# Kernel optimization log

Measured on AMD Instinct MI355X. Metric: run time of the kernel, lower is better.

Reference implementation:

```python
import jax, jax.numpy as jnp
import numpy as np

N = 100000
E = 1600000
IN_FT = 128
OUT_FT = 128
SELF_LOOP_FILL = 3.0


def setup_inputs() -> dict:
    key = jax.random.key(0)
    k1, k2, k3, k4 = jax.random.split(key, 4)
    seq = jax.random.normal(k1, (N, IN_FT), dtype=jnp.float32)
    edge_index = jax.random.randint(k2, (2, E), 0, N, dtype=jnp.int64)
    edge_weight = jax.random.uniform(k3, (E,), dtype=jnp.float32)
    # xavier_uniform for Linear(in_ft, out_ft): W shape [out_ft, in_ft]
    limit = float(np.sqrt(6.0 / (IN_FT + OUT_FT)))
    W = jax.random.uniform(k4, (OUT_FT, IN_FT), dtype=jnp.float32, minval=-limit, maxval=limit)
    return {"seq": seq, "edge_weight": edge_weight, "W": W, "edge_index": edge_index}


def reference(seq, edge_weight, W, edge_index):
    n = seq.shape[0]
    # dropout with drop_prob=0.0 is identity; fc_1: x = seq @ W^T
    x = seq @ W.T  # [N, out_ft]
    # add self loops with fill_value=3.0
    loops = jnp.arange(n, dtype=edge_index.dtype)
    row = jnp.concatenate([edge_index[0], loops])
    col = jnp.concatenate([edge_index[1], loops])
    w = jnp.concatenate([edge_weight, jnp.full((n,), SELF_LOOP_FILL, dtype=edge_weight.dtype)])
    # symmetric normalization: deg^-1/2 [row] * w * deg^-1/2 [col]
    deg = jax.ops.segment_sum(w, row, num_segments=n)
    deg_inv_sqrt = jnp.where(deg > 0, jax.lax.rsqrt(deg), jnp.zeros_like(deg))
    norm = deg_inv_sqrt[row] * w * deg_inv_sqrt[col]
    # sparse aggregation: out[r] += norm_e * x[c]
    out = jax.ops.segment_sum(norm[:, None] * x[col], row, num_segments=n)
    return jax.nn.relu(out)
```

## Files before the change

### kernel.cpp

```cpp
#include <hip/hip_runtime.h>


#define TPB 256
#define NBROWS 256
#define BCAP 4608
#define RCAP 48
#define EPB 2048
#define GPW 4

typedef __attribute__((ext_vector_type(8))) short s16x8;
typedef __attribute__((ext_vector_type(4))) float f32x4;

__device__ inline unsigned bf16rne(float x) {
    unsigned u = __float_as_uint(x);
    u += 0x7FFF + ((u >> 16) & 1);
    return u >> 16;
}

__global__ void k_init(int* __restrict__ cursor, int m,
                       const float* __restrict__ W, unsigned* __restrict__ wb) {
    int i = blockIdx.x * TPB + threadIdx.x;
    if (i < m) cursor[i] = 0;
    if (i < 2048) {
        int j = i >> 4, g = i & 15;
        const float* src = W + j * 128 + g * 8;
        float4 f0 = *(const float4*)src;
        float4 f1 = *(const float4*)(src + 4);
        uint4 pk;
        pk.x = bf16rne(f0.x) | (bf16rne(f0.y) << 16);
        pk.y = bf16rne(f0.z) | (bf16rne(f0.w) << 16);
        pk.z = bf16rne(f1.x) | (bf16rne(f1.y) << 16);
        pk.w = bf16rne(f1.z) | (bf16rne(f1.w) << 16);
        ((uint4*)wb)[i] = pk;
    }
}

__global__ __launch_bounds__(TPB) void k_partition(const int* __restrict__ ei,
                                                   const float* __restrict__ ew,
                                                   int* __restrict__ cursor,
                                                   int2* __restrict__ part,
                                                   int e, int nb) {
    __shared__ int hist[512];
    __shared__ int chunk[512];
    int t = threadIdx.x;
    hist[t] = 0; hist[t + 256] = 0;
    chunk[t] = 0; chunk[t + 256] = 0;
    __syncthreads();

    long base = (long)blockIdx.x * EPB;
    for (int j = 0; j < EPB / 256; ++j) {
        long idx = base + j * 256 + t;
        if (idx < e) atomicAdd(&hist[ei[idx] >> 8], 1);
    }
    __syncthreads();
    for (int b = t; b < nb; b += TPB) {
        int h = hist[b];
        chunk[b] = (h > 0) ? atomicAdd(&cursor[b * 16], h) : 0;
    }
    __syncthreads();
    hist[t] = 0; hist[t + 256] = 0;
    __syncthreads();
    for (int j = 0; j < EPB / 256; ++j) {
        long idx = base + j * 256 + t;
        if (idx < e) {
            int r = ei[idx];
            int c = ei[e + idx];
            float w = ew[idx];
            int b = r >> 8;
            int rank = atomicAdd(&hist[b], 1);
            int dst = chunk[b] + rank;
            if (dst < BCAP)
                part[(long)b * BCAP + dst] =
                    make_int2(((r & 255) << 17) | c, __float_as_int(w));
        }
    }
}

__global__ __launch_bounds__(TPB) void k_build_prescale(const int2* __restrict__ part,
                                                        const int* __restrict__ cursor,
                                                        unsigned* __restrict__ slotsG,
                                                        float2* __restrict__ dc,
                                                        const float* __restrict__ seq,
                                                        unsigned* __restrict__ xb, int n) {
    __shared__ unsigned lslot[NBROWS * RCAP];
    __shared__ int rowcnt[NBROWS];
    __shared__ float rdis[NBROWS];
    int b = blockIdx.x, t = threadIdx.x;
    rowcnt[t] = 0;
    for (int j = t; j < NBROWS * RCAP; j += TPB) lslot[j] = 0;
    __syncthreads();

    int m = cursor[b * 16]; if (m > BCAP) m = BCAP;
    for (int i = t; i < m; i += TPB) {
        int2 en = part[(long)b * BCAP + i];
        int rl = ((unsigned)en.x) >> 17;
        int c  = en.x & 0x1FFFF;
        float w = __int_as_float(en.y);
        int pos = atomicAdd(&rowcnt[rl], 1);
        if (pos < RCAP) {
            int q = (int)(w * 32768.0f);
            if (q > 32767) q = 32767;
            lslot[rl * RCAP + pos] = ((unsigned)q << 17) | (unsigned)c;
        }
    }
    __syncthreads();

    int node = b * NBROWS + t;
    float di = 0.0f;
    if (node < n) {
        int rc = rowcnt[t]; if (rc > RCAP) rc = RCAP;
        float s = 0.0f;
        for (int k = 0; k < rc; ++k)
            s += ((float)(lslot[t * RCAP + k] >> 17) + 0.5f) * (1.0f / 32768.0f);
        di = rsqrtf(3.0f + s);
        dc[node] = make_float2(di, __int_as_float(rc));
    }
    rdis[t] = di;
    for (int j = t; j < NBROWS * RCAP; j += TPB)
        slotsG[(long)b * (NBROWS * RCAP) + j] = lslot[j];
    __syncthreads();

    long pbase = (long)b * NBROWS * 64;
    long plim = (long)n * 64;
    for (int j = t; j < NBROWS * 64; j += TPB) {
        long pidx = pbase + j;
        if (pidx < plim) {
            float d = rdis[j >> 6];
            float2 s2 = ((const float2*)seq)[pidx];
            xb[pidx] = bf16rne(d * s2.x) | (bf16rne(d * s2.y) << 16);
        }
    }
}

__global__ __launch_bounds__(TPB) void k_gather_gemm(const unsigned* __restrict__ xb,
                                                     const unsigned* __restrict__ slotsG,
                                                     const float2* __restrict__ dc,
                                                     const unsigned* __restrict__ wb,
                                                     float* __restrict__ out, int n) {
    __shared__ short ylds[16 * 128];
    int t = threadIdx.x;
    int wave = t >> 6, lane = t & 63;

    int node0 = blockIdx.x * (4 * GPW) + wave * GPW;

    float di[GPW];
    int   m[GPW];
    int   cl[GPW];
    float vl[GPW];
    float2 acc[GPW];
    int mmax = 0;

#pragma unroll
    for (int q = 0; q < GPW; ++q) {
        int node = node0 + q;
        bool has = (node < n);
        float2 d = has ? dc[node] : make_float2(0.0f, __int_as_float(0));
        di[q] = d.x;
        m[q] = __float_as_int(d.y);
        if (m[q] > mmax) mmax = m[q];
        unsigned s = (has && lane < m[q]) ? slotsG[(long)node * RCAP + lane] : 0u;
        int c = (int)(s & 0x1FFFF); if (c > n - 1) c = n - 1;
        cl[q] = c;
        vl[q] = (lane < m[q]) ? ((float)(s >> 17) + 0.5f) * (1.0f / 32768.0f) : 0.0f;
        unsigned u = has ? xb[(long)node * 64 + lane] : 0u;
        acc[q].x = 3.0f * __uint_as_float(u << 16);
        acc[q].y = 3.0f * __uint_as_float(u & 0xFFFF0000u);
    }

    unsigned xva[GPW], xvb[GPW], xvc[GPW];
    float    va[GPW],  vb[GPW],  vc[GPW];

#pragma unroll
    for (int q = 0; q < GPW; ++q) {
        int c = __shfl(cl[q], 0);
        va[q] = __shfl(vl[q], 0);
        xva[q] = xb[(long)c * 64 + lane];
    }
#pragma unroll
    for (int q = 0; q < GPW; ++q) {
        int c = __shfl(cl[q], 1);
        vb[q] = __shfl(vl[q], 1);
        xvb[q] = xb[(long)c * 64 + lane];
    }

    for (int p = 0; p < mmax; p += 3) {
#pragma unroll
        for (int q = 0; q < GPW; ++q) {
            int c = __shfl(cl[q], p + 2);
            vc[q] = __shfl(vl[q], p + 2);
            xvc[q] = xb[(long)c * 64 + lane];
        }
#pragma unroll
        for (int q = 0; q < GPW; ++q) {
            acc[q].x = fmaf(va[q], __uint_as_float(xva[q] << 16), acc[q].x);
            acc[q].y = fmaf(va[q], __uint_as_float(xva[q] & 0xFFFF0000u), acc[q].y);
        }
#pragma unroll
        for (int q = 0; q < GPW; ++q) {
            int c = __shfl(cl[q], p + 3);
            va[q] = __shfl(vl[q], p + 3);
            xva[q] = xb[(long)c * 64 + lane];
        }
#pragma unroll
        for (int q = 0; q < GPW; ++q) {
            acc[q].x = fmaf(vb[q], __uint_as_float(xvb[q] << 16), acc[q].x);
            acc[q].y = fmaf(vb[q], __uint_as_float(xvb[q] & 0xFFFF0000u), acc[q].y);
        }
#pragma unroll
        for (int q = 0; q < GPW; ++q) {
            int c = __shfl(cl[q], p + 4);
            vb[q] = __shfl(vl[q], p + 4);
            xvb[q] = xb[(long)c * 64 + lane];
        }
#pragma unroll
        for (int q = 0; q < GPW; ++q) {
            acc[q].x = fmaf(vc[q], __uint_as_float(xvc[q] << 16), acc[q].x);
            acc[q].y = fmaf(vc[q], __uint_as_float(xvc[q] & 0xFFFF0000u), acc[q].y);
        }
    }

    int quad = lane >> 4, l15 = lane & 15;
    s16x8 bfr[2][4];
#pragma unroll
    for (int h = 0; h < 2; ++h)
#pragma unroll
        for (int kc = 0; kc < 4; ++kc)
            bfr[h][kc] = ((const s16x8*)wb)[((wave * 2 + h) * 16 + l15) * 16 + kc * 4 + quad];

#pragma unroll
    for (int q = 0; q < GPW; ++q) {
        int r = wave * GPW + q;
        unsigned pkv = bf16rne(di[q] * acc[q].x) | (bf16rne(di[q] * acc[q].y) << 16);
        ((unsigned*)ylds)[r * 64 + ((((lane >> 2) ^ r) & 15) << 2) + (lane & 3)] = pkv;
    }
    __syncthreads();

    f32x4 acc2[2];
    acc2[0] = (f32x4){0.0f, 0.0f, 0.0f, 0.0f};
    acc2[1] = (f32x4){0.0f, 0.0f, 0.0f, 0.0f};

#pragma unroll
    for (int kc = 0; kc < 4; ++kc) {
        int gA = kc * 4 + quad;
        s16x8 a = *(const s16x8*)&ylds[l15 * 128 + ((gA ^ l15) << 3)];
        acc2[0] = __builtin_amdgcn_mfma_f32_16x16x32_bf16(a, bfr[0][kc], acc2[0], 0, 0, 0);
        acc2[1] = __builtin_amdgcn_mfma_f32_16x16x32_bf16(a, bfr[1][kc], acc2[1], 0, 0, 0);
    }

    long base = (long)blockIdx.x * 16;
#pragma unroll
    for (int h = 0; h < 2; ++h) {
        int ct = wave * 2 + h;
#pragma unroll
        for (int i = 0; i < 4; ++i) {
            long gr = base + quad * 4 + i;
            if (gr < n)
                out[gr * 128 + ct * 16 + l15] = fmaxf(acc2[h][i], 0.0f);
        }
    }
}

extern "C" void kernel_launch(void* const* d_in, const int* in_sizes, int n_in,
                              void* d_out, int out_size, void* d_ws, size_t ws_size,
                              hipStream_t stream) {
    const float* seq = (const float*)d_in[0];
    const float* ew  = (const float*)d_in[1];
    const float* W   = (const float*)d_in[2];
    const int*   ei  = (const int*)d_in[3];
    float* out = (float*)d_out;

    int n = in_sizes[0] / 128;
    int e = in_sizes[1];
    int nb = (n + NBROWS - 1) / NBROWS;

    char* w8 = (char*)d_ws;
    unsigned* xb   = (unsigned*)w8;
    size_t off = (size_t)n * 64 * 4;
    int2* part     = (int2*)(w8 + off);
    off += (size_t)nb * BCAP * 8;
    unsigned* slotsG = (unsigned*)(w8 + off);
    off += (size_t)nb * NBROWS * RCAP * 4;
    int* cursor    = (int*)(w8 + off);
    off += (size_t)nb * 16 * 4;
    float2* dc     = (float2*)(w8 + off);
    off += (size_t)n * 8;
    unsigned* wb   = (unsigned*)(w8 + off);

    k_init          <<<(nb * 16 + TPB - 1) / TPB, TPB, 0, stream>>>(cursor, nb * 16, W, wb);
    k_partition     <<<(e + EPB - 1) / EPB, TPB, 0, stream>>>(ei, ew, cursor, part, e, nb);
    k_build_prescale<<<nb, TPB, 0, stream>>>(part, cursor, slotsG, dc, seq, xb, n);
    k_gather_gemm   <<<(n + 4 * GPW - 1) / (4 * GPW), TPB, 0, stream>>>(xb, slotsG, dc, wb, out, n);
}
```

Measured before the change: 280.9 us.

## Replace two-level bucket partition with direct global-atomic scatter into per-row slots

Removes the bucket histogram/partition pass and the shared-memory slot build. Each edge now does a global atomicAdd on a per-row counter and writes its packed slot straight into a per-row RCAP array. A new wave-per-node kernel reduces the degree with shuffles and prescales seq into bf16. The change cuts one kernel launch and one round-trip through the intermediate partition buffer, at the cost of many contended global atomics and scattered writes. Slot ordering within a row also becomes nondeterministic.

```diff
diff --git a/kernel.cpp b/kernel.cpp
--- a/kernel.cpp
+++ b/kernel.cpp
@@ -2,10 +2,7 @@
 
 
 #define TPB 256
-#define NBROWS 256
-#define BCAP 4608
 #define RCAP 48
-#define EPB 2048
 #define GPW 4
 
 typedef __attribute__((ext_vector_type(8))) short s16x8;
@@ -17,11 +14,15 @@
     return u >> 16;
 }
 
-__global__ void k_init(int* __restrict__ cursor, int m,
-                       const float* __restrict__ W, unsigned* __restrict__ wb) {
-    int i = blockIdx.x * TPB + threadIdx.x;
-    if (i < m) cursor[i] = 0;
-    if (i < 2048) {
+__global__ __launch_bounds__(TPB) void k_scatter(const int* __restrict__ ei,
+                                                 const float* __restrict__ ew,
+                                                 int* __restrict__ rowcnt,
+                                                 unsigned* __restrict__ slotsG,
+                                                 const float* __restrict__ W,
+                                                 unsigned* __restrict__ wb, int e) {
+    int t = threadIdx.x;
+    if (blockIdx.x < 8) {
+        int i = blockIdx.x * TPB + t;
         int j = i >> 4, g = i & 15;
         const float* src = W + j * 128 + g * 8;
         float4 f0 = *(const float4*)src;
@@ -33,103 +34,43 @@
         pk.w = bf16rne(f1.z) | (bf16rne(f1.w) << 16);
         ((uint4*)wb)[i] = pk;
     }
-}
-
-__global__ __launch_bounds__(TPB) void k_partition(const int* __restrict__ ei,
-                                                   const float* __restrict__ ew,
-                                                   int* __restrict__ cursor,
-                                                   int2* __restrict__ part,
-                                                   int e, int nb) {
-    __shared__ int hist[512];
-    __shared__ int chunk[512];
-    int t = threadIdx.x;
-    hist[t] = 0; hist[t + 256] = 0;
-    chunk[t] = 0; chunk[t + 256] = 0;
-    __syncthreads();
-
-    long base = (long)blockIdx.x * EPB;
-    for (int j = 0; j < EPB / 256; ++j) {
-        long idx = base + j * 256 + t;
-        if (idx < e) atomicAdd(&hist[ei[idx] >> 8], 1);
-    }
-    __syncthreads();
-    for (int b = t; b < nb; b += TPB) {
-        int h = hist[b];
-        chunk[b] = (h > 0) ? atomicAdd(&cursor[b * 16], h) : 0;
-    }
-    __syncthreads();
-    hist[t] = 0; hist[t + 256] = 0;
-    __syncthreads();
-    for (int j = 0; j < EPB / 256; ++j) {
-        long idx = base + j * 256 + t;
-        if (idx < e) {
-            int r = ei[idx];
-            int c = ei[e + idx];
-            float w = ew[idx];
-            int b = r >> 8;
-            int rank = atomicAdd(&hist[b], 1);
-            int dst = chunk[b] + rank;
-            if (dst < BCAP)
-                part[(long)b * BCAP + dst] =
-                    make_int2(((r & 255) << 17) | c, __float_as_int(w));
-        }
-    }
-}
-
-__global__ __launch_bounds__(TPB) void k_build_prescale(const int2* __restrict__ part,
-                                                        const int* __restrict__ cursor,
-                                                        unsigned* __restrict__ slotsG,
-                                                        float2* __restrict__ dc,
-                                                        const float* __restrict__ seq,
-                                                        unsigned* __restrict__ xb, int n) {
-    __shared__ unsigned lslot[NBROWS * RCAP];
-    __shared__ int rowcnt[NBROWS];
-    __shared__ float rdis[NBROWS];
-    int b = blockIdx.x, t = threadIdx.x;
-    rowcnt[t] = 0;
-    for (int j = t; j < NBROWS * RCAP; j += TPB) lslot[j] = 0;
-    __syncthreads();
-
-    int m = cursor[b * 16]; if (m > BCAP) m = BCAP;
-    for (int i = t; i < m; i += TPB) {
-        int2 en = part[(long)b * BCAP + i];
-        int rl = ((unsigned)en.x) >> 17;
-        int c  = en.x & 0x1FFFF;
-        float w = __int_as_float(en.y);
-        int pos = atomicAdd(&rowcnt[rl], 1);
-        if (pos < RCAP) {
-            int q = (int)(w * 32768.0f);
-            if (q > 32767) q = 32767;
-            lslot[rl * RCAP + pos] = ((unsigned)q << 17) | (unsigned)c;
-        }
-    }
-    __syncthreads();
-
-    int node = b * NBROWS + t;
-    float di = 0.0f;
-    if (node < n) {
-        int rc = rowcnt[t]; if (rc > RCAP) rc = RCAP;
-        float s = 0.0f;
-        for (int k = 0; k < rc; ++k)
-            s += ((float)(lslot[t * RCAP + k] >> 17) + 0.5f) * (1.0f / 32768.0f);
-        di = rsqrtf(3.0f + s);
-        dc[node] = make_float2(di, __int_as_float(rc));
-    }
-    rdis[t] = di;
-    for (int j = t; j < NBROWS * RCAP; j += TPB)
-        slotsG[(long)b * (NBROWS * RCAP) + j] = lslot[j];
-    __syncthreads();
-
-    long pbase = (long)b * NBROWS * 64;
-    long plim = (long)n * 64;
-    for (int j = t; j < NBROWS * 64; j += TPB) {
-        long pidx = pbase + j;
-        if (pidx < plim) {
-            float d = rdis[j >> 6];
-            float2 s2 = ((const float2*)seq)[pidx];
-            xb[pidx] = bf16rne(d * s2.x) | (bf16rne(d * s2.y) << 16);
-        }
-    }
+    long idx = (long)blockIdx.x * TPB + t;
+    if (idx < e) {
+        int r = ei[idx];
+        int c = ei[e + idx];
+        float w = ew[idx];
+        int q = (int)(w * 32768.0f);
+        if (q > 32767) q = 32767;
+        int pos = atomicAdd(&rowcnt[r], 1);
+        if (pos < RCAP)
+            slotsG[(long)r * RCAP + pos] = ((unsigned)q << 17) | (unsigned)c;
+    }
+}
+
+__global__ __launch_bounds__(TPB) void k_disprescale(const unsigned* __restrict__ slotsG,
+                                                     const int* __restrict__ rowcnt,
+                                                     const float* __restrict__ seq,
+                                                     float2* __restrict__ dc,
+                                                     unsigned* __restrict__ xb, int n) {
+    int wave = threadIdx.x >> 6, lane = threadIdx.x & 63;
+    int node = blockIdx.x * 4 + wave;
+    if (node >= n) return;
+
+    int rc = rowcnt[node]; if (rc > RCAP) rc = RCAP;
+    float v = 0.0f;
+    if (lane < rc) {
+        unsigned s = slotsG[(long)node * RCAP + lane];
+        v = ((float)(s >> 17) + 0.5f) * (1.0f / 32768.0f);
+    }
+    v += __shfl_xor(v, 1);  v += __shfl_xor(v, 2);
+    v += __shfl_xor(v, 4);  v += __shfl_xor(v, 8);
+    v += __shfl_xor(v, 16); v += __shfl_xor(v, 32);
+    float di = rsqrtf(3.0f + v);
+    if (lane == 0) dc[node] = make_float2(di, __int_as_float(rc));
+
+    long p = (long)node * 64 + lane;
+    float2 s2 = ((const float2*)seq)[p];
+    xb[p] = bf16rne(di * s2.x) | (bf16rne(di * s2.y) << 16);
 }
 
 __global__ __launch_bounds__(TPB) void k_gather_gemm(const unsigned* __restrict__ xb,
@@ -271,23 +212,20 @@
 
     int n = in_sizes[0] / 128;
     int e = in_sizes[1];
-    int nb = (n + NBROWS - 1) / NBROWS;
 
     char* w8 = (char*)d_ws;
-    unsigned* xb   = (unsigned*)w8;
+    unsigned* xb     = (unsigned*)w8;
     size_t off = (size_t)n * 64 * 4;
-    int2* part     = (int2*)(w8 + off);
-    off += (size_t)nb * BCAP * 8;
     unsigned* slotsG = (unsigned*)(w8 + off);
-    off += (size_t)nb * NBROWS * RCAP * 4;
-    int* cursor    = (int*)(w8 + off);
-    off += (size_t)nb * 16 * 4;
-    float2* dc     = (float2*)(w8 + off);
+    off += (size_t)n * RCAP * 4;
+    int* rowcnt      = (int*)(w8 + off);
+    off += (size_t)n * 4;
+    float2* dc       = (float2*)(w8 + off);
     off += (size_t)n * 8;
-    unsigned* wb   = (unsigned*)(w8 + off);
-
-    k_init          <<<(nb * 16 + TPB - 1) / TPB, TPB, 0, stream>>>(cursor, nb * 16, W, wb);
-    k_partition     <<<(e + EPB - 1) / EPB, TPB, 0, stream>>>(ei, ew, cursor, part, e, nb);
-    k_build_prescale<<<nb, TPB, 0, stream>>>(part, cursor, slotsG, dc, seq, xb, n);
-    k_gather_gemm   <<<(n + 4 * GPW - 1) / (4 * GPW), TPB, 0, stream>>>(xb, slotsG, dc, wb, out, n);
-}
+    unsigned* wb     = (unsigned*)(w8 + off);
+
+    hipMemsetAsync(rowcnt, 0, (size_t)n * 4, stream);
+    k_scatter     <<<(e + TPB - 1) / TPB, TPB, 0, stream>>>(ei, ew, rowcnt, slotsG, W, wb, e);
+    k_disprescale <<<(n + 3) / 4, TPB, 0, stream>>>(slotsG, rowcnt, seq, dc, xb, n);
+    k_gather_gemm <<<(n + 4 * GPW - 1) / (4 * GPW), TPB, 0, stream>>>(xb, slotsG, dc, wb, out, n);
+}
```

New measurement: 309.4 us. 1.1x slower.
